# Kernel optimization log

Measured on AMD Instinct MI355X. Metric: run time of the kernel, lower is better.

The kernel has to match this reference:

```python
import jax, jax.numpy as jnp
import numpy as np

N_ENV = 100000
D_PS = 512
N_SPECIES = 4
N_SUPPORT = 256
N_STRUCT = 1000
ZETA = 2


def setup_inputs() -> dict:
    key = jax.random.key(0)
    k1, k2, k3, k4, k5 = jax.random.split(key, 5)
    power_spectrum = jax.random.normal(k1, (N_ENV, D_PS), dtype=jnp.float32)
    sp = jax.random.normal(k2, (N_SPECIES, N_SUPPORT, D_PS), dtype=jnp.float32)
    # CosineKernel asserts support points are unit-norm
    support_points = sp / jnp.linalg.norm(sp, axis=-1, keepdims=True)
    weights = jax.random.normal(k3, (N_SPECIES, 1, N_SUPPORT), dtype=jnp.float32)
    all_species = jax.random.randint(k4, (N_ENV,), 0, N_SPECIES, dtype=jnp.int64)
    structure_ids = jnp.sort(jax.random.randint(k5, (N_ENV,), 0, N_STRUCT, dtype=jnp.int64))
    return {
        "power_spectrum": power_spectrum,
        "support_points": support_points,
        "weights": weights,
        "all_species": all_species,
        "structure_ids": structure_ids,
    }


def reference(power_spectrum, support_points, weights, all_species, structure_ids):
    # Normalize each environment's power spectrum (CosineKernel)
    ps = power_spectrum / jnp.linalg.norm(power_spectrum, axis=1, keepdims=True)
    # Kernel of every environment against every species' support set: [N, S, M]
    k = jnp.einsum("nd,smd->nsm", ps, support_points) ** ZETA
    # Per-row energy contribution for each species: k @ weights[s].T -> [N, S]
    contrib = jnp.einsum("nsm,sm->ns", k, weights[:, 0, :])
    # Species masking: each row only contributes through its own species' kernel
    onehot = jax.nn.one_hot(all_species, N_SPECIES, dtype=contrib.dtype)  # [N, S]
    per_row = jnp.sum(contrib * onehot, axis=1)  # [N]
    # Segmented sum over structures (equivalent to looping over structures_slices)
    energy = jax.ops.segment_sum(per_row, structure_ids, num_segments=N_STRUCT)
    return energy[:, None]  # [n_structures, 1]
```

## Files before the change

### kernel.cpp

```cpp
#include <hip/hip_runtime.h>
#include <hip/hip_bf16.h>


constexpr int kNEnv     = 100000;
constexpr int kDPS      = 512;
constexpr int kNSpecies = 4;
constexpr int kNSupport = 256;
constexpr int kCap      = 32768;

constexpr int BN = 64;
constexpr int BK = 32;

typedef __attribute__((ext_vector_type(8))) short short8;
typedef __attribute__((ext_vector_type(4))) float f32x4;

__device__ __forceinline__ short8 pack_bf16x8(const float4& a, const float4& b) {
  union { short8 v; __hip_bfloat162 h[4]; } u;
  u.h[0] = __float22bfloat162_rn({a.x, a.y});
  u.h[1] = __float22bfloat162_rn({a.z, a.w});
  u.h[2] = __float22bfloat162_rn({b.x, b.y});
  u.h[3] = __float22bfloat162_rn({b.z, b.w});
  return u.v;
}

__global__ void scatter_convert_kernel(const float* __restrict__ sp,
                                       const int* __restrict__ species,
                                       const int* __restrict__ sid,
                                       int* __restrict__ cnt, int* __restrict__ perm,
                                       int* __restrict__ sidp, short* __restrict__ spb) {
  const int t = threadIdx.x;
  const int b = blockIdx.x;
  if (b < (kNSpecies * kNSupport * kDPS) / (256 * 8)) {
    const int base = (b * 256 + t) * 8;
    const float4 lo = *(const float4*)(sp + base);
    const float4 hi = *(const float4*)(sp + base + 4);
    *(short8*)(spb + base) = pack_bf16x8(lo, hi);
  }
  __shared__ int lcnt[kNSpecies];
  __shared__ int lbase[kNSpecies];
  if (t < kNSpecies) lcnt[t] = 0;
  __syncthreads();
  const int i = b * 256 + t;
  const bool v = i < kNEnv;
  int s = 0, r = 0, g = 0;
  if (v) { s = species[i]; r = atomicAdd(&lcnt[s], 1); g = sid[i]; }
  __syncthreads();
  if (t < kNSpecies) lbase[t] = lcnt[t] ? atomicAdd(&cnt[t], lcnt[t]) : 0;
  __syncthreads();
  if (v) {
    const int d = s * kCap + lbase[s] + r;
    perm[d] = i;
    sidp[d] = g;
  }
}

__global__ __launch_bounds__(256, 3) void gap_gemm_kernel(
    const float* __restrict__ ps, const short* __restrict__ spb,
    const float* __restrict__ w, const int* __restrict__ cnt,
    const int* __restrict__ perm, const int* __restrict__ sidp,
    float* __restrict__ energy) {
  const int s     = blockIdx.z;
  const int count = min(cnt[s], kCap);
  const int tile0 = blockIdx.x * BN;
  if (tile0 >= count) return;

  __shared__ float red[4][64];
  __shared__ float sqs[BN];

  const int tid  = threadIdx.x;
  const int wv   = tid >> 6;
  const int lane = tid & 63;
  const int l15  = lane & 15;
  const int lq   = lane >> 4;

  const float* aptr[4];
  #pragma unroll
  for (int fi = 0; fi < 4; ++fi) {
    const int ge   = tile0 + fi * 16 + l15;
    const int arow = perm[s * kCap + (ge < count ? ge : count - 1)];
    aptr[fi] = ps + (size_t)arow * kDPS + lq * 8;
  }
  const short* bptr[4];
  float wgt[4];
  const float* w_s = w + s * kNSupport;
  #pragma unroll
  for (int fj = 0; fj < 4; ++fj) {
    const int m = wv * 64 + fj * 16 + l15;
    bptr[fj] = spb + ((size_t)s * kNSupport + m) * kDPS + lq * 8;
    wgt[fj]  = w_s[m];
  }

  f32x4 acc[4][4];
  #pragma unroll
  for (int fi = 0; fi < 4; ++fi)
    #pragma unroll
    for (int fj = 0; fj < 4; ++fj) acc[fi][fj] = (f32x4)0.f;
  float sq[4] = {0.f, 0.f, 0.f, 0.f};

  #pragma unroll 4
  for (int k0 = 0; k0 < kDPS; k0 += BK) {
    short8 bf[4];
    #pragma unroll
    for (int fj = 0; fj < 4; ++fj) bf[fj] = *(const short8*)(bptr[fj] + k0);
    #pragma unroll
    for (int fi = 0; fi < 4; ++fi) {
      const float4 lo = *(const float4*)(aptr[fi] + k0);
      const float4 hi = *(const float4*)(aptr[fi] + k0 + 4);
      sq[fi] += lo.x * lo.x + lo.y * lo.y + lo.z * lo.z + lo.w * lo.w
              + hi.x * hi.x + hi.y * hi.y + hi.z * hi.z + hi.w * hi.w;
      const short8 af = pack_bf16x8(lo, hi);
      #pragma unroll
      for (int fj = 0; fj < 4; ++fj)
        acc[fi][fj] = __builtin_amdgcn_mfma_f32_16x16x32_bf16(af, bf[fj], acc[fi][fj], 0, 0, 0);
    }
  }

  if (wv == 0) {
    #pragma unroll
    for (int fi = 0; fi < 4; ++fi) {
      float p = sq[fi];
      p += __shfl_xor(p, 16, 64);
      p += __shfl_xor(p, 32, 64);
      if (lane < 16) sqs[fi * 16 + lane] = p;
    }
  }

  #pragma unroll
  for (int fi = 0; fi < 4; ++fi) {
    #pragma unroll
    for (int r = 0; r < 4; ++r) {
      float p = 0.f;
      #pragma unroll
      for (int fj = 0; fj < 4; ++fj) {
        const float c = acc[fi][fj][r];
        p += c * c * wgt[fj];
      }
      p += __shfl_xor(p, 1, 64);
      p += __shfl_xor(p, 2, 64);
      p += __shfl_xor(p, 4, 64);
      p += __shfl_xor(p, 8, 64);
      if (l15 == 0) red[wv][fi * 16 + lq * 4 + r] = p;
    }
  }
  __syncthreads();
  if (tid < BN) {
    const float v = red[0][tid] + red[1][tid] + red[2][tid] + red[3][tid];
    const int g  = tile0 + tid;
    if (g < count) atomicAdd(&energy[sidp[s * kCap + g]], v / sqs[tid]);
  }
}

extern "C" void kernel_launch(void* const* d_in, const int* in_sizes, int n_in,
                              void* d_out, int out_size, void* d_ws, size_t ws_size,
                              hipStream_t stream) {
  const float* ps      = (const float*)d_in[0];
  const float* sp      = (const float*)d_in[1];
  const float* w       = (const float*)d_in[2];
  const int*   species = (const int*)d_in[3];
  const int*   sid     = (const int*)d_in[4];
  float* energy = (float*)d_out;

  char* wsb  = (char*)d_ws;
  int*   cnt  = (int*)wsb;
  int*   perm = (int*)(wsb + 256);
  int*   sidp = (int*)(wsb + 256 + 4 * kCap * sizeof(int));
  short* spb  = (short*)(wsb + 256 + 8 * kCap * sizeof(int));

  hipMemsetAsync(cnt, 0, 16, stream);
  hipMemsetAsync(energy, 0, out_size * sizeof(float), stream);

  scatter_convert_kernel<<<(kNEnv + 255) / 256, 256, 0, stream>>>(
      sp, species, sid, cnt, perm, sidp, spb);

  dim3 grid(kCap / BN, 1, kNSpecies);
  gap_gemm_kernel<<<grid, 256, 0, stream>>>(ps, spb, w, cnt, perm, sidp, energy);
}
```

Before: 405.0 us.

## Stage gathered A rows through double-buffered LDS via direct global-to-LDS loads

Before, each wave loaded its own gathered power-spectrum rows straight from global memory, so all four waves read the same A data four times. Now the tile of A rows is loaded once per block into a swizzled LDS buffer using global_load_lds, double-buffered so the next K-slice loads while the current one feeds the MFMAs. Only wave 0 accumulates the row norms. This removes the redundant global reads and hides gather latency, at the cost of LDS usage, block barriers each K-step, and a stricter swizzle/address scheme that has to map correctly onto the MFMA operand layout.

```diff
diff --git a/kernel.cpp b/kernel.cpp
--- a/kernel.cpp
+++ b/kernel.cpp
@@ -21,6 +21,12 @@
   u.h[2] = __float22bfloat162_rn({b.x, b.y});
   u.h[3] = __float22bfloat162_rn({b.z, b.w});
   return u.v;
+}
+
+__device__ __forceinline__ void gload_lds16(const float* g, float* l) {
+  __builtin_amdgcn_global_load_lds(
+      (const __attribute__((address_space(1))) void*)g,
+      (__attribute__((address_space(3))) void*)l, 16, 0, 0);
 }
 
 __global__ void scatter_convert_kernel(const float* __restrict__ sp,
@@ -64,7 +70,8 @@
   const int tile0 = blockIdx.x * BN;
   if (tile0 >= count) return;
 
-  __shared__ float red[4][64];
+  __shared__ float a_lds[2][BN * BK];
+  __shared__ float red[4][BN];
   __shared__ float sqs[BN];
 
   const int tid  = threadIdx.x;
@@ -73,13 +80,18 @@
   const int l15  = lane & 15;
   const int lq   = lane >> 4;
 
-  const float* aptr[4];
-  #pragma unroll
-  for (int fi = 0; fi < 4; ++fi) {
-    const int ge   = tile0 + fi * 16 + l15;
-    const int arow = perm[s * kCap + (ge < count ? ge : count - 1)];
-    aptr[fi] = ps + (size_t)arow * kDPS + lq * 8;
-  }
+  const int sby = (((lane & 7) << 4) ^ ((lane >> 3) << 4));
+  const float* ssrc[2];
+  #pragma unroll
+  for (int c = 0; c < 2; ++c) {
+    int r  = wv * 16 + c * 8 + (lane >> 3);
+    int ge = tile0 + r;
+    ge = ge < count ? ge : count - 1;
+    ssrc[c] = ps + (size_t)perm[s * kCap + ge] * kDPS + (sby >> 2);
+  }
+  const int dof0 = (wv * 16) * BK;
+  const int dof1 = (wv * 16 + 8) * BK;
+
   const short* bptr[4];
   float wgt[4];
   const float* w_s = w + s * kNSupport;
@@ -90,6 +102,11 @@
     wgt[fj]  = w_s[m];
   }
 
+  const int fswz = (l15 & 7) << 4;
+  const int cb1  = (lq * 32) ^ fswz;
+  const int cb2  = (lq * 32 + 16) ^ fswz;
+  const int rowb = l15 * 128;
+
   f32x4 acc[4][4];
   #pragma unroll
   for (int fi = 0; fi < 4; ++fi)
@@ -97,23 +114,46 @@
     for (int fj = 0; fj < 4; ++fj) acc[fi][fj] = (f32x4)0.f;
   float sq[4] = {0.f, 0.f, 0.f, 0.f};
 
-  #pragma unroll 4
-  for (int k0 = 0; k0 < kDPS; k0 += BK) {
-    short8 bf[4];
-    #pragma unroll
-    for (int fj = 0; fj < 4; ++fj) bf[fj] = *(const short8*)(bptr[fj] + k0);
-    #pragma unroll
-    for (int fi = 0; fi < 4; ++fi) {
-      const float4 lo = *(const float4*)(aptr[fi] + k0);
-      const float4 hi = *(const float4*)(aptr[fi] + k0 + 4);
-      sq[fi] += lo.x * lo.x + lo.y * lo.y + lo.z * lo.z + lo.w * lo.w
-              + hi.x * hi.x + hi.y * hi.y + hi.z * hi.z + hi.w * hi.w;
-      const short8 af = pack_bf16x8(lo, hi);
-      #pragma unroll
-      for (int fj = 0; fj < 4; ++fj)
-        acc[fi][fj] = __builtin_amdgcn_mfma_f32_16x16x32_bf16(af, bf[fj], acc[fi][fj], 0, 0, 0);
-    }
-  }
+#define STAGE(BUF, K0) do {                        \
+    gload_lds16(ssrc[0] + (K0), &a_lds[BUF][dof0]); \
+    gload_lds16(ssrc[1] + (K0), &a_lds[BUF][dof1]); \
+  } while (0)
+
+#define BODY(BUF, K0) do {                                                      \
+    short8 bf[4];                                                               \
+    _Pragma("unroll")                                                           \
+    for (int fj = 0; fj < 4; ++fj) bf[fj] = *(const short8*)(bptr[fj] + (K0));  \
+    const char* abase = (const char*)&a_lds[BUF][0];                            \
+    _Pragma("unroll")                                                           \
+    for (int fi = 0; fi < 4; ++fi) {                                            \
+      const float4 f1 = *(const float4*)(abase + fi * 2048 + rowb + cb1);       \
+      const float4 f2 = *(const float4*)(abase + fi * 2048 + rowb + cb2);       \
+      if (wv == 0)                                                              \
+        sq[fi] += f1.x * f1.x + f1.y * f1.y + f1.z * f1.z + f1.w * f1.w         \
+                + f2.x * f2.x + f2.y * f2.y + f2.z * f2.z + f2.w * f2.w;        \
+      const short8 af = pack_bf16x8(f1, f2);                                    \
+      _Pragma("unroll")                                                         \
+      for (int fj = 0; fj < 4; ++fj)                                            \
+        acc[fi][fj] =                                                           \
+            __builtin_amdgcn_mfma_f32_16x16x32_bf16(af, bf[fj], acc[fi][fj], 0, 0, 0); \
+    }                                                                           \
+  } while (0)
+
+  STAGE(0, 0);
+  __syncthreads();
+
+  #pragma unroll 1
+  for (int kp = 0; kp < kDPS; kp += 2 * BK) {
+    STAGE(1, kp + BK);
+    BODY(0, kp);
+    __syncthreads();
+    if (kp + 2 * BK < kDPS) STAGE(0, kp + 2 * BK);
+    BODY(1, kp + BK);
+    __syncthreads();
+  }
+
+#undef STAGE
+#undef BODY
 
   if (wv == 0) {
     #pragma unroll
```

After: 347.0 us. 14.3% less time.
